# Optimization experiments

Hardware: AMD Instinct MI355X
Metric: run time of the kernel (lower is better)

## Reference

```python
import jax, jax.numpy as jnp
import numpy as np

# Lloyd-Max (Max 1960) optimal 16-level quantizer for N(0,1), bits=4
_CODEBOOK_4 = np.array([-2.7326, -2.069, -1.6181, -1.2562, -0.9424, -0.6568,
                        -0.3881, -0.1284, 0.1284, 0.3881, 0.6568, 0.9424,
                        1.2562, 1.6181, 2.069, 2.7326], dtype=np.float32)
DIM = 256


def setup_inputs() -> dict:
    key = jax.random.key(0)
    kx, kq = jax.random.split(key)
    x = jax.random.normal(kx, (4, 4096, DIM), dtype=jnp.float32)
    # orthogonal rotation via QR of a Gaussian matrix (mirrors torch.linalg.qr)
    rotation, _ = jnp.linalg.qr(jax.random.normal(kq, (DIM, DIM), dtype=jnp.float32))
    codebook = jnp.asarray(_CODEBOOK_4)
    return {"x": x, "rotation": rotation, "codebook": codebook}


def reference(x, rotation, codebook):
    shape = x.shape
    d = shape[-1]
    sqrt_d = jnp.sqrt(jnp.asarray(d, dtype=x.dtype))
    x_flat = x.reshape(-1, d)                                   # (N, d)
    x_norm = jnp.maximum(
        jnp.linalg.norm(x_flat, axis=-1, keepdims=True), 1e-8)  # (N, 1)
    u = x_flat / x_norm                                         # unit vectors
    y_scaled = (u @ rotation.T) * sqrt_d                        # ~N(0,1) coords
    # nearest codebook entry per scalar coordinate: (N, d, K) -> argmin over K
    idx = jnp.argmin(jnp.abs(y_scaled[..., None] - codebook), axis=-1)
    y_hat = codebook[idx] / sqrt_d                              # (N, d)
    x_hat = (y_hat @ rotation) * x_norm                         # de-rotate, rescale
    return x_hat.reshape(shape)
```

## Files before the change

kernel.cpp:

```cpp
#include <hip/hip_runtime.h>

typedef _Float16 f16;
typedef _Float16 f16x4 __attribute__((ext_vector_type(4)));
typedef _Float16 f16x8 __attribute__((ext_vector_type(8)));
typedef float f32x16 __attribute__((ext_vector_type(16)));
typedef float f32x4 __attribute__((ext_vector_type(4)));

#define APITCH 264
#define WREG 67584

__global__ __launch_bounds__(512) void prep_kernel(const float* __restrict__ R,
                                                   f16* __restrict__ ws) {
  __shared__ float Lrs[32][260];
  const int b = blockIdx.x;
  const int g = b >> 2, h = b & 3;
  const int t = threadIdx.x;
  f16* W1h = ws;
  f16* W1l = ws + WREG;
  f16* W2h = ws + 2 * WREG;

  #pragma unroll
  for (int it = 0; it < 4; ++it) {
    int c = it * 512 + t;
    int row = c >> 6, c4 = (c & 63) * 4;
    f32x4 v = *(const f32x4*)&R[(long)(32 * g + row) * 256 + c4];
    *(f32x4*)&Lrs[row][c4] = v;
  }
  __syncthreads();

  if (t < 256) {
    int f_loc = 4 * h + (t >> 6), l = t & 63;
    int k0 = 16 * f_loc + 8 * (l >> 5);
    const float* src = &Lrs[l & 31][k0];
    f16x8 hi, lo;
    #pragma unroll
    for (int j = 0; j < 8; ++j) {
      float v = src[j] * 256.0f;
      f16 hh = (f16)v;
      hi[j] = hh;
      lo[j] = (f16)(v - (float)hh);
    }
    long o = (long)(g * 16 + f_loc) * 512 + l * 8;
    *(f16x8*)(W1h + o) = hi;
    *(f16x8*)(W1l + o) = lo;
  } else {
    int u = t - 256;
    int gp = 2 * h + (u >> 7), e = (u >> 6) & 1, l = u & 63;
    int lr0 = 16 * e + 8 * (l >> 5);
    int col = 32 * gp + (l & 31);
    f16x8 hv;
    #pragma unroll
    for (int j = 0; j < 8; ++j) hv[j] = (f16)Lrs[lr0 + j][col];
    long o = (long)(gp * 16 + 2 * g + e) * 512 + l * 8;
    *(f16x8*)(W2h + o) = hv;
  }
}

__device__ __forceinline__ float rfl(float x) {
  return __builtin_bit_cast(float,
      __builtin_amdgcn_readfirstlane(__builtin_bit_cast(int, x)));
}

__global__ __launch_bounds__(512, 4) void tq_main(
    const float* __restrict__ X, const float* __restrict__ CB,
    const f16* __restrict__ ws, float* __restrict__ OUT) {
  __shared__ f16 A1h[64][APITCH];
  __shared__ f16 A1l[64][APITCH];
  __shared__ float s2s[64];

  const int tid = threadIdx.x;
  const int lane = tid & 63;
  const int wv = tid >> 6;
  const int lrow = lane & 31;
  const int kg = lane >> 5;
  const long row0 = (long)blockIdx.x * 64;

  const f16* W1h = ws;
  const f16* W1l = ws + WREG;
  const f16* W2h = ws + 2 * WREG;

  const int r = tid >> 3, q = tid & 7;
  const float* xp = X + (row0 + r) * 256 + q * 32;
  float xa[32];
  #pragma unroll
  for (int i = 0; i < 8; ++i) {
    f32x4 v = ((const f32x4*)xp)[i];
    xa[4 * i] = v.x; xa[4 * i + 1] = v.y; xa[4 * i + 2] = v.z; xa[4 * i + 3] = v.w;
  }

  const f16* W1hp = W1h + (long)(wv * 16) * 512 + lane * 8;
  const f16* W1lp = W1l + (long)(wv * 16) * 512 + lane * 8;
  f16x8 bh0 = *(const f16x8*)(W1hp);
  f16x8 bl0 = *(const f16x8*)(W1lp);
  f16x8 bh1 = *(const f16x8*)(W1hp + 512);
  f16x8 bl1 = *(const f16x8*)(W1lp + 512);

  float cbf[16];
  #pragma unroll
  for (int i = 0; i < 16; ++i) cbf[i] = rfl(CB[i]);

  float ss = 0.f;
  #pragma unroll
  for (int i = 0; i < 32; ++i) ss += xa[i] * xa[i];
  ss += __shfl_xor(ss, 4, 8);
  ss += __shfl_xor(ss, 2, 8);
  ss += __shfl_xor(ss, 1, 8);
  float nrm = fmaxf(sqrtf(ss), 1e-8f);
  float s1f = 4096.0f / nrm;
  if (q == 0) s2s[r] = nrm * 0.0625f;

  #pragma unroll
  for (int c8 = 0; c8 < 4; ++c8) {
    f16x8 h, l;
    #pragma unroll
    for (int j = 0; j < 8; ++j) {
      float a = xa[c8 * 8 + j] * s1f;
      f16 hh = (f16)a;
      h[j] = hh;
      l[j] = (f16)(a - (float)hh);
    }
    *(f16x8*)&A1h[r][q * 32 + c8 * 8] = h;
    *(f16x8*)&A1l[r][q * 32 + c8 * 8] = l;
  }
  __syncthreads();

  f32x16 zv;
  #pragma unroll
  for (int i = 0; i < 16; ++i) zv[i] = 0.0f;
  f32x16 acc0 = zv, acc1 = zv;

#define MM1_STAGE(BH, BL, KS)                                                   \
  {                                                                             \
    const int k0 = (KS) * 16 + kg * 8;                                          \
    f16x8 ah0 = *(const f16x8*)&A1h[lrow][k0];                                  \
    f16x8 al0 = *(const f16x8*)&A1l[lrow][k0];                                  \
    f16x8 ah1 = *(const f16x8*)&A1h[32 + lrow][k0];                             \
    f16x8 al1 = *(const f16x8*)&A1l[32 + lrow][k0];                             \
    acc0 = __builtin_amdgcn_mfma_f32_32x32x16_f16(ah0, BH, acc0, 0, 0, 0);      \
    acc1 = __builtin_amdgcn_mfma_f32_32x32x16_f16(ah1, BH, acc1, 0, 0, 0);      \
    acc0 = __builtin_amdgcn_mfma_f32_32x32x16_f16(al0, BH, acc0, 0, 0, 0);      \
    acc1 = __builtin_amdgcn_mfma_f32_32x32x16_f16(al1, BH, acc1, 0, 0, 0);      \
    acc0 = __builtin_amdgcn_mfma_f32_32x32x16_f16(ah0, BL, acc0, 0, 0, 0);      \
    acc1 = __builtin_amdgcn_mfma_f32_32x32x16_f16(ah1, BL, acc1, 0, 0, 0);      \
    BH = *(const f16x8*)(W1hp + ((KS) + 2) * 512);                              \
    BL = *(const f16x8*)(W1lp + ((KS) + 2) * 512);                              \
  }

  #pragma unroll
  for (int ksb = 0; ksb < 16; ksb += 2) {
    MM1_STAGE(bh0, bl0, ksb)
    MM1_STAGE(bh1, bl1, ksb + 1)
  }
#undef MM1_STAGE

  const f16* W2p = W2h + (long)(wv * 16) * 512 + lane * 8;
  f16x8 c0 = *(const f16x8*)(W2p);
  f16x8 c1 = *(const f16x8*)(W2p + 512);

  float M[15];
  #pragma unroll
  for (int t = 0; t < 15; ++t) M[t] = 65536.0f * (0.5f * (cbf[t] + cbf[t + 1]));
  unsigned int cpk[8];
  #pragma unroll
  for (int i = 0; i < 8; ++i) {
    unsigned short lb = __builtin_bit_cast(unsigned short, (f16)cbf[2 * i]);
    unsigned short hb = __builtin_bit_cast(unsigned short, (f16)cbf[2 * i + 1]);
    cpk[i] = ((unsigned int)hb << 16) | (unsigned int)lb;
  }

  __syncthreads();

  f16 (*Qs)[APITCH] = A1h;
#define QUANT(ACC, MOFF)                                                        \
  _Pragma("unroll")                                                             \
  for (int rr = 0; rr < 16; ++rr) {                                             \
    float y = ACC[rr];                                                          \
    int row = (MOFF) + 4 * kg + (rr & 3) + 8 * (rr >> 2);                       \
    int kk = 32 * wv + lrow;                                                    \
    bool b3 = y > M[7];                                                         \
    float m2 = b3 ? M[11] : M[3];                                               \
    bool b2 = y > m2;                                                           \
    float m1 = b3 ? (b2 ? M[13] : M[9]) : (b2 ? M[5] : M[1]);                   \
    bool b1 = y > m1;                                                           \
    float m0 = b1 ? (b3 ? (b2 ? M[14] : M[10]) : (b2 ? M[6] : M[2]))            \
                  : (b3 ? (b2 ? M[12] : M[8]) : (b2 ? M[4] : M[0]));            \
    bool b0 = y > m0;                                                           \
    unsigned int pp = b3 ? (b2 ? (b1 ? cpk[7] : cpk[6]) : (b1 ? cpk[5] : cpk[4])) \
                         : (b2 ? (b1 ? cpk[3] : cpk[2]) : (b1 ? cpk[1] : cpk[0])); \
    unsigned short qb = (unsigned short)(b0 ? (pp >> 16) : (pp & 0xFFFFu));     \
    Qs[row][kk] = __builtin_bit_cast(f16, qb);                                  \
  }

  QUANT(acc0, 0)
  QUANT(acc1, 32)
#undef QUANT
  __syncthreads();

  f32x16 acc2_0 = zv, acc2_1 = zv;

#define MM2_STAGE(CS, KS)                                                       \
  {                                                                             \
    const int k0 = (KS) * 16 + kg * 8;                                          \
    f16x8 qa0 = *(const f16x8*)&Qs[lrow][k0];                                   \
    f16x8 qa1 = *(const f16x8*)&Qs[32 + lrow][k0];                              \
    acc2_0 = __builtin_amdgcn_mfma_f32_32x32x16_f16(qa0, CS, acc2_0, 0, 0, 0);  \
    acc2_1 = __builtin_amdgcn_mfma_f32_32x32x16_f16(qa1, CS, acc2_1, 0, 0, 0);  \
    CS = *(const f16x8*)(W2p + ((KS) + 2) * 512);                               \
  }

  #pragma unroll
  for (int ksb = 0; ksb < 16; ksb += 2) {
    MM2_STAGE(c0, ksb)
    MM2_STAGE(c1, ksb + 1)
  }
#undef MM2_STAGE

  #pragma unroll
  for (int rr = 0; rr < 16; ++rr) {
    int row = 4 * kg + (rr & 3) + 8 * (rr >> 2);
    int col = 32 * wv + lrow;
    OUT[(row0 + row) * 256 + col] = acc2_0[rr] * s2s[row];
    OUT[(row0 + 32 + row) * 256 + col] = acc2_1[rr] * s2s[32 + row];
  }
}

#define FB_APITCH 264
#define FB_B1PITCH 40
#define FB_B2PITCH 264

__global__ __launch_bounds__(256, 1) void tq_main_fb(
    const float* __restrict__ X, const float* __restrict__ R,
    const float* __restrict__ CB, float* __restrict__ OUT) {
  __shared__ f16 A1h[64][FB_APITCH];
  __shared__ f16 A1l[64][FB_APITCH];
  __shared__ f16 Qs[64][FB_APITCH];
  __shared__ f32x4 Braw[2624];
  __shared__ float pn[4][64];
  __shared__ float s1s[64];
  __shared__ float s2s[64];

  f16 (*B1h)[FB_B1PITCH] = (f16(*)[FB_B1PITCH])Braw;
  f16 (*B1l)[FB_B1PITCH] = (f16(*)[FB_B1PITCH])((char*)Braw + 20480);
  f16 (*B2h)[FB_B2PITCH] = (f16(*)[FB_B2PITCH])Braw;

  const int tid = threadIdx.x;
  const int lane = tid & 63;
  const int wv = tid >> 6;
  const int lrow = lane & 31;
  const int kg = lane >> 5;
  const long row0 = (long)blockIdx.x * 64;

  float cbf[16];
  #pragma unroll
  for (int i = 0; i < 16; ++i) cbf[i] = CB[i];
  float M[15];
  #pragma unroll
  for (int t = 0; t < 15; ++t) M[t] = 65536.0f * (0.5f * (cbf[t] + cbf[t + 1]));
  unsigned int cpk[8];
  #pragma unroll
  for (int i = 0; i < 8; ++i) {
    unsigned short lb = __builtin_bit_cast(unsigned short, (f16)cbf[2 * i]);
    unsigned short hb = __builtin_bit_cast(unsigned short, (f16)cbf[2 * i + 1]);
    cpk[i] = ((unsigned int)hb << 16) | (unsigned int)lb;
  }

  const int xrow = tid >> 2, xq = tid & 3;
  const float* xp = X + (row0 + xrow) * 256 + xq * 64;
  float xa[64];
  #pragma unroll
  for (int i = 0; i < 16; ++i) {
    f32x4 v = ((const f32x4*)xp)[i];
    xa[4 * i] = v.x; xa[4 * i + 1] = v.y; xa[4 * i + 2] = v.z; xa[4 * i + 3] = v.w;
  }
  float ss = 0.f;
  #pragma unroll
  for (int i = 0; i < 64; ++i) ss += xa[i] * xa[i];
  pn[xq][xrow] = ss;
  __syncthreads();
  if (tid < 64) {
    float s = pn[0][tid] + pn[1][tid] + pn[2][tid] + pn[3][tid];
    float nrm = fmaxf(sqrtf(s), 1e-8f);
    s1s[tid] = 4096.0f / nrm;
    s2s[tid] = nrm * 0.0625f;
  }
  __syncthreads();

  {
    float s1f = s1s[xrow];
    #pragma unroll
    for (int c8 = 0; c8 < 8; ++c8) {
      f16x8 h, l;
      #pragma unroll
      for (int j = 0; j < 8; ++j) {
        float a = xa[c8 * 8 + j] * s1f;
        f16 hh = (f16)a;
        h[j] = hh;
        l[j] = (f16)(a - (float)hh);
      }
      *(f16x8*)&A1h[xrow][xq * 64 + c8 * 8] = h;
      *(f16x8*)&A1l[xrow][xq * 64 + c8 * 8] = l;
    }
  }

  f32x4 pf[8];
  #pragma unroll
  for (int q = 0; q < 8; ++q) {
    int c = q * 256 + tid;
    pf[q] = *(const f32x4*)&R[(long)(c >> 3) * 256 + ((c & 7) * 4)];
  }

  f32x16 zv;
  #pragma unroll
  for (int i = 0; i < 16; ++i) zv[i] = 0.0f;
  f32x16 acc[2][2];
  acc[0][0] = zv; acc[0][1] = zv; acc[1][0] = zv; acc[1][1] = zv;

  for (int kp = 0; kp < 8; ++kp) {
    __syncthreads();
    #pragma unroll
    for (int q = 0; q < 8; ++q) {
      int c = q * 256 + tid;
      int n = c >> 3, k4 = (c & 7) * 4;
      f16x4 h, l;
      #pragma unroll
      for (int j = 0; j < 4; ++j) {
        float sv = pf[q][j] * 256.0f;
        f16 hh = (f16)sv;
        h[j] = hh;
        l[j] = (f16)(sv - (float)hh);
      }
      *(f16x4*)&B1h[n][k4] = h;
      *(f16x4*)&B1l[n][k4] = l;
    }
    __syncthreads();
    if (kp < 7) {
      #pragma unroll
      for (int q = 0; q < 8; ++q) {
        int c = q * 256 + tid;
        pf[q] = *(const f32x4*)&R[(long)(c >> 3) * 256 + (kp + 1) * 32 + ((c & 7) * 4)];
      }
    }
    #pragma unroll
    for (int ks = 0; ks < 2; ++ks) {
      const int k0 = kp * 32 + ks * 16 + kg * 8;
      const int lk = ks * 16 + kg * 8;
      f16x8 ah[2], al[2], bhf[2], blf[2];
      #pragma unroll
      for (int m = 0; m < 2; ++m) {
        ah[m] = *(const f16x8*)&A1h[32 * m + lrow][k0];
        al[m] = *(const f16x8*)&A1l[32 * m + lrow][k0];
      }
      #pragma unroll
      for (int n = 0; n < 2; ++n) {
        int col = 64 * wv + 32 * n + lrow;
        bhf[n] = *(const f16x8*)&B1h[col][lk];
        blf[n] = *(const f16x8*)&B1l[col][lk];
      }
      #pragma unroll
      for (int m = 0; m < 2; ++m)
        #pragma unroll
        for (int n = 0; n < 2; ++n) {
          acc[m][n] = __builtin_amdgcn_mfma_f32_32x32x16_f16(ah[m], bhf[n], acc[m][n], 0, 0, 0);
          acc[m][n] = __builtin_amdgcn_mfma_f32_32x32x16_f16(al[m], bhf[n], acc[m][n], 0, 0, 0);
          acc[m][n] = __builtin_amdgcn_mfma_f32_32x32x16_f16(ah[m], blf[n], acc[m][n], 0, 0, 0);
          acc[m][n] = __builtin_amdgcn_mfma_f32_32x32x16_f16(al[m], blf[n], acc[m][n], 0, 0, 0);
        }
    }
  }

  #pragma unroll
  for (int q = 0; q < 8; ++q) {
    int c = q * 256 + tid;
    pf[q] = *(const f32x4*)&R[(long)(c >> 6) * 256 + ((c & 63) * 4)];
  }

  #pragma unroll
  for (int m = 0; m < 2; ++m)
    #pragma unroll
    for (int n = 0; n < 2; ++n)
      #pragma unroll
      for (int rr = 0; rr < 16; ++rr) {
        float y = acc[m][n][rr];
        int row = 32 * m + 4 * kg + (rr & 3) + 8 * (rr >> 2);
        int kk = 64 * wv + 32 * n + lrow;
        bool b3 = y > M[7];
        float m2 = b3 ? M[11] : M[3];
        bool b2 = y > m2;
        float m1 = b3 ? (b2 ? M[13] : M[9]) : (b2 ? M[5] : M[1]);
        bool b1 = y > m1;
        float m0 = b1 ? (b3 ? (b2 ? M[14] : M[10]) : (b2 ? M[6] : M[2]))
                      : (b3 ? (b2 ? M[12] : M[8]) : (b2 ? M[4] : M[0]));
        bool b0 = y > m0;
        unsigned int pp = b3 ? (b2 ? (b1 ? cpk[7] : cpk[6]) : (b1 ? cpk[5] : cpk[4]))
                             : (b2 ? (b1 ? cpk[3] : cpk[2]) : (b1 ? cpk[1] : cpk[0]));
        unsigned short qb = (unsigned short)(b0 ? (pp >> 16) : (pp & 0xFFFFu));
        Qs[row][kk] = __builtin_bit_cast(f16, qb);
      }
  __syncthreads();

  f32x16 acc2[2][2];
  acc2[0][0] = zv; acc2[0][1] = zv; acc2[1][0] = zv; acc2[1][1] = zv;

  for (int kp = 0; kp < 8; ++kp) {
    if (kp) __syncthreads();
    #pragma unroll
    for (int q = 0; q < 8; ++q) {
      int c = q * 256 + tid;
      int k = c >> 6, n4 = (c & 63) * 4;
      f16x4 h;
      #pragma unroll
      for (int j = 0; j < 4; ++j) h[j] = (f16)pf[q][j];
      *(f16x4*)&B2h[k][n4] = h;
    }
    __syncthreads();
    if (kp < 7) {
      #pragma unroll
      for (int q = 0; q < 8; ++q) {
        int c = q * 256 + tid;
        pf[q] = *(const f32x4*)&R[(long)((kp + 1) * 32 + (c >> 6)) * 256 + ((c & 63) * 4)];
      }
    }
    #pragma unroll
    for (int ks = 0; ks < 2; ++ks) {
      const int k0 = kp * 32 + ks * 16 + kg * 8;
      const int lk = ks * 16 + kg * 8;
      f16x8 qa[2], bb[2];
      #pragma unroll
      for (int m = 0; m < 2; ++m) qa[m] = *(const f16x8*)&Qs[32 * m + lrow][k0];
      #pragma unroll
      for (int n = 0; n < 2; ++n) {
        int colg = 64 * wv + 32 * n + lrow;
        #pragma unroll
        for (int j = 0; j < 8; ++j) bb[n][j] = B2h[lk + j][colg];
      }
      #pragma unroll
      for (int m = 0; m < 2; ++m)
        #pragma unroll
        for (int n = 0; n < 2; ++n)
          acc2[m][n] = __builtin_amdgcn_mfma_f32_32x32x16_f16(qa[m], bb[n], acc2[m][n], 0, 0, 0);
    }
  }

  #pragma unroll
  for (int m = 0; m < 2; ++m)
    #pragma unroll
    for (int n = 0; n < 2; ++n)
      #pragma unroll
      for (int rr = 0; rr < 16; ++rr) {
        int row = 32 * m + 4 * kg + (rr & 3) + 8 * (rr >> 2);
        int col = 64 * wv + 32 * n + lrow;
        OUT[(row0 + row) * 256 + col] = acc2[m][n][rr] * s2s[row];
      }
}

extern "C" void kernel_launch(void* const* d_in, const int* in_sizes, int n_in,
                              void* d_out, int out_size, void* d_ws, size_t ws_size,
                              hipStream_t stream) {
  const float* X = (const float*)d_in[0];
  const float* R = (const float*)d_in[1];
  const float* CB = (const float*)d_in[2];
  float* OUT = (float*)d_out;
  const int nrows = in_sizes[0] / 256;

  if (ws_size >= (size_t)3 * WREG * sizeof(f16)) {
    f16* ws = (f16*)d_ws;
    prep_kernel<<<32, 512, 0, stream>>>(R, ws);
    tq_main<<<nrows / 64, 512, 0, stream>>>(X, CB, ws, OUT);
  } else {
    tq_main_fb<<<nrows / 64, 256, 0, stream>>>(X, R, CB, OUT);
  }
}
```

Before: 28.83 us.

## Process two 32-row tiles per block with async LDS staging and register-resident W1

```diff
diff --git a/kernel.cpp b/kernel.cpp
--- a/kernel.cpp
+++ b/kernel.cpp
@@ -61,102 +61,52 @@
       __builtin_amdgcn_readfirstlane(__builtin_bit_cast(int, x)));
 }
 
-__global__ __launch_bounds__(512, 4) void tq_main(
+__global__ __launch_bounds__(512, 2) void tq_main(
     const float* __restrict__ X, const float* __restrict__ CB,
     const f16* __restrict__ ws, float* __restrict__ OUT) {
-  __shared__ f16 A1h[64][APITCH];
-  __shared__ f16 A1l[64][APITCH];
-  __shared__ float s2s[64];
+  __shared__ float Xb0[32][256];
+  __shared__ float Xb1[32][256];
+  __shared__ f16 A1h[32][APITCH];
+  __shared__ f16 A1l[32][APITCH];
+  __shared__ f16 Qs[32][APITCH];
+  __shared__ float s2s[32];
 
   const int tid = threadIdx.x;
   const int lane = tid & 63;
   const int wv = tid >> 6;
   const int lrow = lane & 31;
   const int kg = lane >> 5;
-  const long row0 = (long)blockIdx.x * 64;
+  const long row0a = (long)blockIdx.x * 32;
+  const long row0b = (long)(blockIdx.x + 256) * 32;
 
   const f16* W1h = ws;
   const f16* W1l = ws + WREG;
   const f16* W2h = ws + 2 * WREG;
 
-  const int r = tid >> 3, q = tid & 7;
-  const float* xp = X + (row0 + r) * 256 + q * 32;
-  float xa[32];
-  #pragma unroll
-  for (int i = 0; i < 8; ++i) {
-    f32x4 v = ((const f32x4*)xp)[i];
-    xa[4 * i] = v.x; xa[4 * i + 1] = v.y; xa[4 * i + 2] = v.z; xa[4 * i + 3] = v.w;
-  }
+#define STAGE_X(GROW0, LBUF)                                                    \
+  _Pragma("unroll")                                                             \
+  for (int i = 0; i < 4; ++i) {                                                 \
+    const float* gp = X + (GROW0) * 256 + i * 2048 + wv * 256 + lane * 4;       \
+    float* lp = &LBUF[0][0] + i * 2048 + wv * 256;                              \
+    __builtin_amdgcn_global_load_lds(                                           \
+        (const __attribute__((address_space(1))) void*)gp,                      \
+        (__attribute__((address_space(3))) void*)lp, 16, 0, 0);                 \
+  }
+
+  STAGE_X(row0a, Xb0)
 
   const f16* W1hp = W1h + (long)(wv * 16) * 512 + lane * 8;
   const f16* W1lp = W1l + (long)(wv * 16) * 512 + lane * 8;
-  f16x8 bh0 = *(const f16x8*)(W1hp);
-  f16x8 bl0 = *(const f16x8*)(W1lp);
-  f16x8 bh1 = *(const f16x8*)(W1hp + 512);
-  f16x8 bl1 = *(const f16x8*)(W1lp + 512);
+#define LD_W1(N)                                                                \
+  f16x8 w1h##N = *(const f16x8*)(W1hp + (N) * 512);                             \
+  f16x8 w1l##N = *(const f16x8*)(W1lp + (N) * 512);
+  LD_W1(0) LD_W1(1) LD_W1(2) LD_W1(3) LD_W1(4) LD_W1(5) LD_W1(6) LD_W1(7)
+  LD_W1(8) LD_W1(9) LD_W1(10) LD_W1(11) LD_W1(12) LD_W1(13) LD_W1(14) LD_W1(15)
+#undef LD_W1
 
   float cbf[16];
   #pragma unroll
   for (int i = 0; i < 16; ++i) cbf[i] = rfl(CB[i]);
-
-  float ss = 0.f;
-  #pragma unroll
-  for (int i = 0; i < 32; ++i) ss += xa[i] * xa[i];
-  ss += __shfl_xor(ss, 4, 8);
-  ss += __shfl_xor(ss, 2, 8);
-  ss += __shfl_xor(ss, 1, 8);
-  float nrm = fmaxf(sqrtf(ss), 1e-8f);
-  float s1f = 4096.0f / nrm;
-  if (q == 0) s2s[r] = nrm * 0.0625f;
-
-  #pragma unroll
-  for (int c8 = 0; c8 < 4; ++c8) {
-    f16x8 h, l;
-    #pragma unroll
-    for (int j = 0; j < 8; ++j) {
-      float a = xa[c8 * 8 + j] * s1f;
-      f16 hh = (f16)a;
-      h[j] = hh;
-      l[j] = (f16)(a - (float)hh);
-    }
-    *(f16x8*)&A1h[r][q * 32 + c8 * 8] = h;
-    *(f16x8*)&A1l[r][q * 32 + c8 * 8] = l;
-  }
-  __syncthreads();
-
-  f32x16 zv;
-  #pragma unroll
-  for (int i = 0; i < 16; ++i) zv[i] = 0.0f;
-  f32x16 acc0 = zv, acc1 = zv;
-
-#define MM1_STAGE(BH, BL, KS)                                                   \
-  {                                                                             \
-    const int k0 = (KS) * 16 + kg * 8;                                          \
-    f16x8 ah0 = *(const f16x8*)&A1h[lrow][k0];                                  \
-    f16x8 al0 = *(const f16x8*)&A1l[lrow][k0];                                  \
-    f16x8 ah1 = *(const f16x8*)&A1h[32 + lrow][k0];                             \
-    f16x8 al1 = *(const f16x8*)&A1l[32 + lrow][k0];                             \
-    acc0 = __builtin_amdgcn_mfma_f32_32x32x16_f16(ah0, BH, acc0, 0, 0, 0);      \
-    acc1 = __builtin_amdgcn_mfma_f32_32x32x16_f16(ah1, BH, acc1, 0, 0, 0);      \
-    acc0 = __builtin_amdgcn_mfma_f32_32x32x16_f16(al0, BH, acc0, 0, 0, 0);      \
-    acc1 = __builtin_amdgcn_mfma_f32_32x32x16_f16(al1, BH, acc1, 0, 0, 0);      \
-    acc0 = __builtin_amdgcn_mfma_f32_32x32x16_f16(ah0, BL, acc0, 0, 0, 0);      \
-    acc1 = __builtin_amdgcn_mfma_f32_32x32x16_f16(ah1, BL, acc1, 0, 0, 0);      \
-    BH = *(const f16x8*)(W1hp + ((KS) + 2) * 512);                              \
-    BL = *(const f16x8*)(W1lp + ((KS) + 2) * 512);                              \
-  }
-
-  #pragma unroll
-  for (int ksb = 0; ksb < 16; ksb += 2) {
-    MM1_STAGE(bh0, bl0, ksb)
-    MM1_STAGE(bh1, bl1, ksb + 1)
-  }
-#undef MM1_STAGE
-
-  const f16* W2p = W2h + (long)(wv * 16) * 512 + lane * 8;
-  f16x8 c0 = *(const f16x8*)(W2p);
-  f16x8 c1 = *(const f16x8*)(W2p + 512);
-
   float M[15];
   #pragma unroll
   for (int t = 0; t < 15; ++t) M[t] = 65536.0f * (0.5f * (cbf[t] + cbf[t + 1]));
@@ -168,60 +118,137 @@
     cpk[i] = ((unsigned int)hb << 16) | (unsigned int)lb;
   }
 
+  const f16* W2p = W2h + (long)(wv * 16) * 512 + lane * 8;
+  const int xr = tid >> 4, xq = tid & 15;
+  f32x16 zv;
+  #pragma unroll
+  for (int i = 0; i < 16; ++i) zv[i] = 0.0f;
+
   __syncthreads();
 
-  f16 (*Qs)[APITCH] = A1h;
-#define QUANT(ACC, MOFF)                                                        \
-  _Pragma("unroll")                                                             \
-  for (int rr = 0; rr < 16; ++rr) {                                             \
-    float y = ACC[rr];                                                          \
-    int row = (MOFF) + 4 * kg + (rr & 3) + 8 * (rr >> 2);                       \
-    int kk = 32 * wv + lrow;                                                    \
-    bool b3 = y > M[7];                                                         \
-    float m2 = b3 ? M[11] : M[3];                                               \
-    bool b2 = y > m2;                                                           \
-    float m1 = b3 ? (b2 ? M[13] : M[9]) : (b2 ? M[5] : M[1]);                   \
-    bool b1 = y > m1;                                                           \
-    float m0 = b1 ? (b3 ? (b2 ? M[14] : M[10]) : (b2 ? M[6] : M[2]))            \
-                  : (b3 ? (b2 ? M[12] : M[8]) : (b2 ? M[4] : M[0]));            \
-    bool b0 = y > m0;                                                           \
-    unsigned int pp = b3 ? (b2 ? (b1 ? cpk[7] : cpk[6]) : (b1 ? cpk[5] : cpk[4])) \
-                         : (b2 ? (b1 ? cpk[3] : cpk[2]) : (b1 ? cpk[1] : cpk[0])); \
-    unsigned short qb = (unsigned short)(b0 ? (pp >> 16) : (pp & 0xFFFFu));     \
-    Qs[row][kk] = __builtin_bit_cast(f16, qb);                                  \
-  }
-
-  QUANT(acc0, 0)
-  QUANT(acc1, 32)
-#undef QUANT
-  __syncthreads();
-
-  f32x16 acc2_0 = zv, acc2_1 = zv;
-
-#define MM2_STAGE(CS, KS)                                                       \
+#define DO_TILE(ROW0, XBUF, ISSUE_NEXT, NROW0, NXBUF)                           \
   {                                                                             \
-    const int k0 = (KS) * 16 + kg * 8;                                          \
-    f16x8 qa0 = *(const f16x8*)&Qs[lrow][k0];                                   \
-    f16x8 qa1 = *(const f16x8*)&Qs[32 + lrow][k0];                              \
-    acc2_0 = __builtin_amdgcn_mfma_f32_32x32x16_f16(qa0, CS, acc2_0, 0, 0, 0);  \
-    acc2_1 = __builtin_amdgcn_mfma_f32_32x32x16_f16(qa1, CS, acc2_1, 0, 0, 0);  \
-    CS = *(const f16x8*)(W2p + ((KS) + 2) * 512);                               \
-  }
-
-  #pragma unroll
-  for (int ksb = 0; ksb < 16; ksb += 2) {
-    MM2_STAGE(c0, ksb)
-    MM2_STAGE(c1, ksb + 1)
-  }
-#undef MM2_STAGE
-
-  #pragma unroll
-  for (int rr = 0; rr < 16; ++rr) {
-    int row = 4 * kg + (rr & 3) + 8 * (rr >> 2);
-    int col = 32 * wv + lrow;
-    OUT[(row0 + row) * 256 + col] = acc2_0[rr] * s2s[row];
-    OUT[(row0 + 32 + row) * 256 + col] = acc2_1[rr] * s2s[32 + row];
-  }
+                                                     \
+    float ss = 0.f;                                                             \
+    _Pragma("unroll")                                                           \
+    for (int i = 0; i < 4; ++i) {                                               \
+      f32x4 v = *(const f32x4*)&XBUF[xr][xq * 16 + i * 4];                      \
+      ss += v.x * v.x + v.y * v.y + v.z * v.z + v.w * v.w;                      \
+    }                                                                           \
+    ss += __shfl_xor(ss, 8, 16);                                                \
+    ss += __shfl_xor(ss, 4, 16);                                                \
+    ss += __shfl_xor(ss, 2, 16);                                                \
+    ss += __shfl_xor(ss, 1, 16);                                                \
+    float nrm = fmaxf(sqrtf(ss), 1e-8f);                                        \
+    float s1f = 4096.0f / nrm;                                                  \
+    if (xq == 0) s2s[xr] = nrm * 0.0625f;                                       \
+                                                                \
+    _Pragma("unroll")                                                           \
+    for (int c8 = 0; c8 < 2; ++c8) {                                            \
+      f32x4 va = *(const f32x4*)&XBUF[xr][xq * 16 + c8 * 8];                    \
+      f32x4 vb = *(const f32x4*)&XBUF[xr][xq * 16 + c8 * 8 + 4];                \
+      f16x8 h, l;                                                               \
+      _Pragma("unroll")                                                         \
+      for (int j = 0; j < 4; ++j) {                                             \
+        float a = va[j] * s1f;                                                  \
+        f16 hh = (f16)a;                                                        \
+        h[j] = hh;                                                              \
+        l[j] = (f16)(a - (float)hh);                                            \
+      }                                                                         \
+      _Pragma("unroll")                                                         \
+      for (int j = 0; j < 4; ++j) {                                             \
+        float a = vb[j] * s1f;                                                  \
+        f16 hh = (f16)a;                                                        \
+        h[4 + j] = hh;                                                          \
+        l[4 + j] = (f16)(a - (float)hh);                                        \
+      }                                                                         \
+      *(f16x8*)&A1h[xr][xq * 16 + c8 * 8] = h;                                  \
+      *(f16x8*)&A1l[xr][xq * 16 + c8 * 8] = l;                                  \
+    }                                                                           \
+    if (ISSUE_NEXT) { STAGE_X(NROW0, NXBUF) }                                   \
+    __syncthreads();                                         \
+                          \
+    f32x16 accH = zv, accL = zv, accM = zv;                                     \
+    MM1_STAGE(0) MM1_STAGE(1) MM1_STAGE(2) MM1_STAGE(3)                         \
+    MM1_STAGE(4) MM1_STAGE(5) MM1_STAGE(6) MM1_STAGE(7)                         \
+    MM1_STAGE(8) MM1_STAGE(9) MM1_STAGE(10) MM1_STAGE(11)                       \
+    MM1_STAGE(12) MM1_STAGE(13) MM1_STAGE(14) MM1_STAGE(15)                     \
+                                \
+    f16x8 c0 = *(const f16x8*)(W2p);                                            \
+    f16x8 c1 = *(const f16x8*)(W2p + 512);                                      \
+    f16x8 c2 = *(const f16x8*)(W2p + 1024);                                     \
+    f16x8 c3 = *(const f16x8*)(W2p + 1536);                                     \
+                                                            \
+    _Pragma("unroll")                                                           \
+    for (int rr = 0; rr < 16; ++rr) {                                           \
+      float y = accH[rr] + accL[rr] + accM[rr];                                 \
+      int row = 4 * kg + (rr & 3) + 8 * (rr >> 2);                              \
+      int kk = 32 * wv + lrow;                                                  \
+      bool b3 = y > M[7];                                                       \
+      float m2 = b3 ? M[11] : M[3];                                             \
+      bool b2 = y > m2;                                                         \
+      float m1 = b3 ? (b2 ? M[13] : M[9]) : (b2 ? M[5] : M[1]);                 \
+      bool b1 = y > m1;                                                         \
+      float m0 = b1 ? (b3 ? (b2 ? M[14] : M[10]) : (b2 ? M[6] : M[2]))          \
+                    : (b3 ? (b2 ? M[12] : M[8]) : (b2 ? M[4] : M[0]));          \
+      bool b0 = y > m0;                                                         \
+      unsigned int pp = b3 ? (b2 ? (b1 ? cpk[7] : cpk[6]) : (b1 ? cpk[5] : cpk[4])) \
+                           : (b2 ? (b1 ? cpk[3] : cpk[2]) : (b1 ? cpk[1] : cpk[0])); \
+      unsigned short qb = (unsigned short)(b0 ? (pp >> 16) : (pp & 0xFFFFu));   \
+      Qs[row][kk] = __builtin_bit_cast(f16, qb);                                \
+    }                                                                           \
+    __syncthreads();                                        \
+                                       \
+    f32x16 acc2 = zv;                                                           \
+    _Pragma("unroll")                                                           \
+    for (int ks = 0; ks < 16; ks += 4) {                                        \
+      {                                                                         \
+        f16x8 qa = *(const f16x8*)&Qs[lrow][ks * 16 + kg * 8];                  \
+        acc2 = __builtin_amdgcn_mfma_f32_32x32x16_f16(qa, c0, acc2, 0, 0, 0);   \
+        c0 = *(const f16x8*)(W2p + (ks + 4) * 512);                             \
+      }                                                                         \
+      {                                                                         \
+        f16x8 qa = *(const f16x8*)&Qs[lrow][(ks + 1) * 16 + kg * 8];            \
+        acc2 = __builtin_amdgcn_mfma_f32_32x32x16_f16(qa, c1, acc2, 0, 0, 0);   \
+        c1 = *(const f16x8*)(W2p + (ks + 5) * 512);                             \
+      }                                                                         \
+      {                                                                         \
+        f16x8 qa = *(const f16x8*)&Qs[lrow][(ks + 2) * 16 + kg * 8];            \
+        acc2 = __builtin_amdgcn_mfma_f32_32x32x16_f16(qa, c2, acc2, 0, 0, 0);   \
+        c2 = *(const f16x8*)(W2p + (ks + 6) * 512);                             \
+      }                                                                         \
+      {                                                                         \
+        f16x8 qa = *(const f16x8*)&Qs[lrow][(ks + 3) * 16 + kg * 8];            \
+        acc2 = __builtin_amdgcn_mfma_f32_32x32x16_f16(qa, c3, acc2, 0, 0, 0);   \
+        c3 = *(const f16x8*)(W2p + (ks + 7) * 512);                             \
+      }                                                                         \
+    }                                                                           \
+                                                                  \
+    _Pragma("unroll")                                                           \
+    for (int rr = 0; rr < 16; ++rr) {                                           \
+      int row = 4 * kg + (rr & 3) + 8 * (rr >> 2);                              \
+      int col = 32 * wv + lrow;                                                 \
+      OUT[((ROW0) + row) * 256 + col] = acc2[rr] * s2s[row];                    \
+    }                                                                           \
+    __syncthreads();     \
+  }
+
+#define MM1_STAGE(N)                                                            \
+  {                                                                             \
+    const int k0 = (N) * 16 + kg * 8;                                           \
+    f16x8 ah = *(const f16x8*)&A1h[lrow][k0];                                   \
+    f16x8 al = *(const f16x8*)&A1l[lrow][k0];                                   \
+    accH = __builtin_amdgcn_mfma_f32_32x32x16_f16(ah, w1h##N, accH, 0, 0, 0);   \
+    accL = __builtin_amdgcn_mfma_f32_32x32x16_f16(al, w1h##N, accL, 0, 0, 0);   \
+    accM = __builtin_amdgcn_mfma_f32_32x32x16_f16(ah, w1l##N, accM, 0, 0, 0);   \
+  }
+
+  DO_TILE(row0a, Xb0, 1, row0b, Xb1)
+  DO_TILE(row0b, Xb1, 0, row0b, Xb1)
+
+#undef MM1_STAGE
+#undef DO_TILE
+#undef STAGE_X
 }
 
 #define FB_APITCH 264
```

After: 30.07 us. +4.3%, slower.
